# Performance work log

Measured on AMD Instinct MI355X. Metric: run time of the kernel, lower is better.

## Reference

```python
import jax, jax.numpy as jnp
import numpy as np

B, T, I, H, O = 4096, 512, 1, 50, 1


def setup_inputs() -> dict:
    key = jax.random.key(0)
    ks = jax.random.split(key, 7)
    s = 1.0 / np.sqrt(H)  # torch LSTM/Linear default init scale
    x = jax.random.normal(ks[0], (B, T, I), dtype=jnp.float32)
    W_ih = jax.random.uniform(ks[1], (4 * H, I), jnp.float32, -s, s)
    W_hh = jax.random.uniform(ks[2], (4 * H, H), jnp.float32, -s, s)
    b_ih = jax.random.uniform(ks[3], (4 * H,), jnp.float32, -s, s)
    b_hh = jax.random.uniform(ks[4], (4 * H,), jnp.float32, -s, s)
    W_fc = jax.random.uniform(ks[5], (O, H), jnp.float32, -s, s)
    b_fc = jax.random.uniform(ks[6], (O,), jnp.float32, -s, s)
    return {"x": x, "W_ih": W_ih, "W_hh": W_hh, "b_ih": b_ih,
            "b_hh": b_hh, "W_fc": W_fc, "b_fc": b_fc}


def reference(x, W_ih, W_hh, b_ih, b_hh, W_fc, b_fc):
    # x: [B, T, I]. Precompute input projections for all timesteps: [B, T, 4H]
    xp = jnp.einsum('bti,gi->btg', x, W_ih) + (b_ih + b_hh)

    def step(carry, xt):
        h, c = carry  # [B, H] each
        gates = xt + h @ W_hh.T  # [B, 4H]; torch gate order: i, f, g, o
        i, f, g, o = jnp.split(gates, 4, axis=-1)
        c = jax.nn.sigmoid(f) * c + jax.nn.sigmoid(i) * jnp.tanh(g)
        h = jax.nn.sigmoid(o) * jnp.tanh(c)
        return (h, c), None

    h0 = jnp.zeros((x.shape[0], W_hh.shape[1]), x.dtype)
    (h_last, _), _ = jax.lax.scan(step, (h0, h0), jnp.swapaxes(xp, 0, 1))
    # final-timestep hidden -> Linear
    return h_last @ W_fc.T + b_fc  # [B, O]
```

## Files before the change

kernel.cpp:

```cpp
#include <hip/hip_runtime.h>
#include <math.h>

#define T_LEN 512
#define H_DIM 50
#define BPB   16
#define NW    13
#define L2E   1.44269504088896f
#define XSTR  520

typedef _Float16 half8_t __attribute__((ext_vector_type(8)));
typedef float    f32x4_t __attribute__((ext_vector_type(4)));

__device__ __forceinline__ f32x4_t mfma16(half8_t a, half8_t b, f32x4_t c) {
#if defined(__HIP_DEVICE_COMPILE__)
    return __builtin_amdgcn_mfma_f32_16x16x32_f16(a, b, c, 0, 0, 0);
#else
    return c;
#endif
}
__device__ __forceinline__ int pk16(float a, float b) {
    return __builtin_bit_cast(int, __builtin_amdgcn_cvt_pkrtz(a, b));
}

__global__ __launch_bounds__(NW * 64, 1) void lstm_mfma(
    const float* __restrict__ x,
    const float* __restrict__ W_ih,
    const float* __restrict__ W_hh,
    const float* __restrict__ b_ih,
    const float* __restrict__ b_hh,
    const float* __restrict__ W_fc,
    const float* __restrict__ b_fc,
    float* __restrict__ out)
{
    const int tid = threadIdx.x;
    const int w   = tid >> 6;
    const int L   = tid & 63;
    const int col = L & 15;
    const int g4  = L >> 4;

    __shared__ _Float16 xls[BPB][XSTR];
    __shared__ __align__(16) _Float16 hb[2][8][BPB][8];

    {
        const float4* xg4 = reinterpret_cast<const float4*>(
            x + (size_t)blockIdx.x * BPB * T_LEN);
        for (int f = tid; f < BPB * T_LEN / 4; f += NW * 64) {
            const float4 v = xg4[f];
            const int bb = f >> 7;
            const int c0 = (f & 127) << 2;
            *reinterpret_cast<int*>(&xls[bb][c0])     = pk16(v.x, v.y);
            *reinterpret_cast<int*>(&xls[bb][c0 + 2]) = pk16(v.z, v.w);
        }
    }
    for (int i = tid; i < 1024; i += NW * 64) reinterpret_cast<int*>(hb)[i] = 0;
    __syncthreads();
    if (tid < BPB) hb[0][6][tid][2] = xls[tid][0];

    const int pA = 16 * w + col;
    const int uA = pA >> 2, gA = pA & 3;
    const float sA = (gA == 2) ? (-2.0f * L2E) : (-L2E);
    half8_t a0, a1;
    #pragma unroll
    for (int j = 0; j < 8; ++j) {
        const int k0 = 8 * g4 + j;
        const int k1 = 32 + k0;
        float v0 = 0.0f, v1 = 0.0f;
        if (uA < H_DIM) {
            const int r = gA * H_DIM + uA;
            v0 = W_hh[r * H_DIM + k0];
            if (k1 < H_DIM)       v1 = W_hh[r * H_DIM + k1];
            else if (k1 == H_DIM) v1 = W_ih[r];
        }
        a0[j] = (_Float16)(v0 * sA);
        a1[j] = (_Float16)(v1 * sA);
    }

    const int uD  = 4 * w + g4;
    const bool wr = (uD < H_DIM);
    f32x4_t biasC;
    #pragma unroll
    for (int j = 0; j < 4; ++j) {
        const float sj = (j == 2) ? (-2.0f * L2E) : (-L2E);
        biasC[j] = wr ? (b_ih[j * H_DIM + uD] + b_hh[j * H_DIM + uD]) * sj : 0.0f;
    }

    const int uDw = wr ? uD : (52 + (uD & 1));
    _Float16* hw = &hb[0][uDw >> 3][col][uDw & 7];
    const _Float16* rB = &hb[0][0][0][0] + (g4 * 128 + col * 8);
    const _Float16* xq = &xls[col][1];
    _Float16* xd = &hb[0][6][col][2];
    const bool xw = (w == 9) && (g4 == 3);

    float c = 0.0f;
    __syncthreads();

    auto step = [&](int RO, int WO, int XI) {
        const half8_t b0 = *reinterpret_cast<const half8_t*>(rB + RO);
        const half8_t b1 = *reinterpret_cast<const half8_t*>(rB + RO + 512);
        _Float16 xn = (_Float16)0.0f;
        if (xw) xn = xq[XI];
        f32x4_t acc = mfma16(a0, b0, biasC);
        acc = mfma16(a1, b1, acc);
        const float ig = __builtin_amdgcn_rcpf(1.0f + __builtin_amdgcn_exp2f(acc[0]));
        const float fg = __builtin_amdgcn_rcpf(1.0f + __builtin_amdgcn_exp2f(acc[1]));
        const float g2 = __builtin_amdgcn_rcpf(1.0f + __builtin_amdgcn_exp2f(acc[2]));
        const float og = __builtin_amdgcn_rcpf(1.0f + __builtin_amdgcn_exp2f(acc[3]));
        const float gt = __fmaf_rn(g2, 2.0f, -1.0f);
        c = __fmaf_rn(fg, c, ig * gt);
        const float et = __builtin_amdgcn_exp2f(c * (-2.0f * L2E));
        const float tc = __fmaf_rn(__builtin_amdgcn_rcpf(1.0f + et), 2.0f, -1.0f);
        const float hv = og * tc;
        hw[WO] = (_Float16)hv;
        if (xw) xd[WO] = xn;
        __syncthreads();
    };

    for (int t = 0; t < T_LEN; t += 4) {
        step(0,    1024, 0);
        step(1024, 0,    1);
        step(0,    1024, 2);
        step(1024, 0,    3);
        xq += 4;
    }

    if (w == 0) {
        float part = 0.0f;
        #pragma unroll
        for (int j = 0; j < 13; ++j) {
            const int u = 13 * g4 + j;
            if (u < H_DIM)
                part += (float)hb[0][u >> 3][col][u & 7] * W_fc[u];
        }
        part += __shfl_xor(part, 16);
        part += __shfl_xor(part, 32);
        if (L < BPB) out[blockIdx.x * BPB + L] = part + b_fc[0];
    }
}

extern "C" void kernel_launch(void* const* d_in, const int* in_sizes, int n_in,
                              void* d_out, int out_size, void* d_ws, size_t ws_size,
                              hipStream_t stream) {
    const float* x    = (const float*)d_in[0];
    const float* W_ih = (const float*)d_in[1];
    const float* W_hh = (const float*)d_in[2];
    const float* b_ih = (const float*)d_in[3];
    const float* b_hh = (const float*)d_in[4];
    const float* W_fc = (const float*)d_in[5];
    const float* b_fc = (const float*)d_in[6];
    float* out = (float*)d_out;

    const int B = in_sizes[0] / T_LEN;
    lstm_mfma<<<dim3(B / BPB), dim3(NW * 64), 0, stream>>>(
        x, W_ih, W_hh, b_ih, b_hh, W_fc, b_fc, out);
}
```

Before: 190.3 us.

## Use 12 waves with the last wave handling two tiles, and merge gate reciprocals

Cuts the workgroup from 13 to 12 waves, so wave 11 now computes an extra MFMA tile for hidden units 48-51. The gate nonlinearities are rewritten so sigmoid(i)*tanh(g) and sigmoid(o)*tanh(c) each take a single reciprocal of a product, which removes several rcp instructions per step. The aim is less barrier cost and fewer transcendental ops per step. The price is a load imbalance: wave 11 now does twice the work on the critical path of every step. Merging the reciprocals also carries some overflow risk when the exponentials are large.

```diff
diff --git a/kernel.cpp b/kernel.cpp
--- a/kernel.cpp
+++ b/kernel.cpp
@@ -4,7 +4,7 @@
 #define T_LEN 512
 #define H_DIM 50
 #define BPB   16
-#define NW    13
+#define NW    12
 #define L2E   1.44269504088896f
 #define XSTR  520
 
@@ -56,61 +56,83 @@
     __syncthreads();
     if (tid < BPB) hb[0][6][tid][2] = xls[tid][0];
 
-    const int pA = 16 * w + col;
-    const int uA = pA >> 2, gA = pA & 3;
-    const float sA = (gA == 2) ? (-2.0f * L2E) : (-L2E);
-    half8_t a0, a1;
-    #pragma unroll
-    for (int j = 0; j < 8; ++j) {
-        const int k0 = 8 * g4 + j;
-        const int k1 = 32 + k0;
-        float v0 = 0.0f, v1 = 0.0f;
-        if (uA < H_DIM) {
-            const int r = gA * H_DIM + uA;
-            v0 = W_hh[r * H_DIM + k0];
-            if (k1 < H_DIM)       v1 = W_hh[r * H_DIM + k1];
-            else if (k1 == H_DIM) v1 = W_ih[r];
+    auto load_pair = [&](int p, half8_t& f0, half8_t& f1) {
+        const int uA = p >> 2, gA = p & 3;
+        const float sA = (gA == 2) ? (-2.0f * L2E) : (-L2E);
+        #pragma unroll
+        for (int j = 0; j < 8; ++j) {
+            const int k0 = 8 * g4 + j;
+            const int k1 = 32 + k0;
+            float v0 = 0.0f, v1 = 0.0f;
+            if (uA < H_DIM) {
+                const int r = gA * H_DIM + uA;
+                v0 = W_hh[r * H_DIM + k0];
+                if (k1 < H_DIM)       v1 = W_hh[r * H_DIM + k1];
+                else if (k1 == H_DIM) v1 = W_ih[r];
+            }
+            f0[j] = (_Float16)(v0 * sA);
+            f1[j] = (_Float16)(v1 * sA);
         }
-        a0[j] = (_Float16)(v0 * sA);
-        a1[j] = (_Float16)(v1 * sA);
-    }
+    };
+    half8_t a0, a1, a20, a21;
+    load_pair(16 * w + col, a0, a1);
+    load_pair(192 + col, a20, a21);
 
-    const int uD  = 4 * w + g4;
-    const bool wr = (uD < H_DIM);
-    f32x4_t biasC;
-    #pragma unroll
-    for (int j = 0; j < 4; ++j) {
-        const float sj = (j == 2) ? (-2.0f * L2E) : (-L2E);
-        biasC[j] = wr ? (b_ih[j * H_DIM + uD] + b_hh[j * H_DIM + uD]) * sj : 0.0f;
-    }
+    auto load_bias = [&](int uD) -> f32x4_t {
+        f32x4_t bc;
+        #pragma unroll
+        for (int j = 0; j < 4; ++j) {
+            const float sj = (j == 2) ? (-2.0f * L2E) : (-L2E);
+            bc[j] = (uD < H_DIM)
+                  ? (b_ih[j * H_DIM + uD] + b_hh[j * H_DIM + uD]) * sj : 0.0f;
+        }
+        return bc;
+    };
+    const int uD1 = 4 * w + g4;
+    const int uD2 = 48 + g4;
+    const f32x4_t biasC1 = load_bias(uD1);
+    const f32x4_t biasC2 = load_bias(uD2);
 
-    const int uDw = wr ? uD : (52 + (uD & 1));
-    _Float16* hw = &hb[0][uDw >> 3][col][uDw & 7];
+    const int uD2w = (uD2 < H_DIM) ? uD2 : (52 + (uD2 & 1));
+    _Float16* hw1 = &hb[0][uD1 >> 3][col][uD1 & 7];
+    _Float16* hw2 = &hb[0][uD2w >> 3][col][uD2w & 7];
     const _Float16* rB = &hb[0][0][0][0] + (g4 * 128 + col * 8);
     const _Float16* xq = &xls[col][1];
     _Float16* xd = &hb[0][6][col][2];
-    const bool xw = (w == 9) && (g4 == 3);
+    const bool xw  = (w == 9) && (g4 == 3);
+    const bool two = (w == 11);
 
-    float c = 0.0f;
+    float c1 = 0.0f, c2 = 0.0f;
     __syncthreads();
+
+    auto update = [&](const f32x4_t& acc, float& c, _Float16* hw, int WO) {
+        const float Ei = __builtin_amdgcn_exp2f(acc[0]);
+        const float Ef = __builtin_amdgcn_exp2f(acc[1]);
+        const float Eg = __builtin_amdgcn_exp2f(acc[2]);
+        const float Eo = __builtin_amdgcn_exp2f(acc[3]);
+        const float fg  = __builtin_amdgcn_rcpf(1.0f + Ef);
+        const float r1  = __builtin_amdgcn_rcpf((1.0f + Ei) * (1.0f + Eg));
+        const float pig = (1.0f - Eg) * r1;
+        c = __fmaf_rn(fg, c, pig);
+        const float Ec = __builtin_amdgcn_exp2f(c * (-2.0f * L2E));
+        const float r2 = __builtin_amdgcn_rcpf((1.0f + Ec) * (1.0f + Eo));
+        const float hv = (1.0f - Ec) * r2;
+        hw[WO] = (_Float16)hv;
+    };
 
     auto step = [&](int RO, int WO, int XI) {
         const half8_t b0 = *reinterpret_cast<const half8_t*>(rB + RO);
         const half8_t b1 = *reinterpret_cast<const half8_t*>(rB + RO + 512);
         _Float16 xn = (_Float16)0.0f;
         if (xw) xn = xq[XI];
-        f32x4_t acc = mfma16(a0, b0, biasC);
+        f32x4_t acc = mfma16(a0, b0, biasC1);
         acc = mfma16(a1, b1, acc);
-        const float ig = __builtin_amdgcn_rcpf(1.0f + __builtin_amdgcn_exp2f(acc[0]));
-        const float fg = __builtin_amdgcn_rcpf(1.0f + __builtin_amdgcn_exp2f(acc[1]));
-        const float g2 = __builtin_amdgcn_rcpf(1.0f + __builtin_amdgcn_exp2f(acc[2]));
-        const float og = __builtin_amdgcn_rcpf(1.0f + __builtin_amdgcn_exp2f(acc[3]));
-        const float gt = __fmaf_rn(g2, 2.0f, -1.0f);
-        c = __fmaf_rn(fg, c, ig * gt);
-        const float et = __builtin_amdgcn_exp2f(c * (-2.0f * L2E));
-        const float tc = __fmaf_rn(__builtin_amdgcn_rcpf(1.0f + et), 2.0f, -1.0f);
-        const float hv = og * tc;
-        hw[WO] = (_Float16)hv;
+        update(acc, c1, hw1, WO);
+        if (two) {
+            f32x4_t acc2 = mfma16(a20, b0, biasC2);
+            acc2 = mfma16(a21, b1, acc2);
+            update(acc2, c2, hw2, WO);
+        }
         if (xw) xd[WO] = xn;
         __syncthreads();
     };
```

After: 194.2 us, median of 2. +2.1%, slower.
